# Performance work log

Hardware: AMD Instinct MI355X
Metric: run time of the kernel (lower is better)

The kernel has to match this reference:

```python
import jax, jax.numpy as jnp
import numpy as np

B, N, D, H, LH, AH = 4, 2048, 512, 4, 64, 64
NUM_BUCKETS = 128
EPS = 1e-6
LENGTHS = np.array([2048, 1536, 1024, 1792])  # jagged per-sequence lengths, sum = 6400


def _ln(x, eps=EPS):
    # F.layer_norm without affine params (biased variance)
    m = jnp.mean(x, axis=-1, keepdims=True)
    v = jnp.var(x, axis=-1, keepdims=True)
    return (x - m) * jax.lax.rsqrt(v + eps)


def _rel_bias(all_timestamps, ts_w):
    # bucketed time-delta relative attention bias -> [B, N, N]
    delta = (all_timestamps[:, :, None] - all_timestamps[:, None, :]).astype(jnp.float32)
    bucket = jnp.clip(jnp.floor(jnp.log1p(jnp.abs(delta))).astype(jnp.int32), 0, NUM_BUCKETS)
    return ts_w[bucket]


def setup_inputs() -> dict:
    key = jax.random.key(0)
    ks = jax.random.split(key, 6)
    offsets = np.concatenate([[0], np.cumsum(LENGTHS)]).astype(np.int32)
    T = int(offsets[-1])
    token_batch = np.repeat(np.arange(B), LENGTHS).astype(np.int32)
    token_pos = np.concatenate([np.arange(l) for l in LENGTHS]).astype(np.int32)
    x = jax.random.normal(ks[0], (T, D), jnp.float32)
    uvqk = jax.random.normal(ks[1], (D, 2 * LH * H + 2 * AH * H), jnp.float32) * 0.02
    o_w = jax.random.normal(ks[2], (D, LH * H), jnp.float32) * 0.02  # torch Linear weight [out, in]
    o_b = jnp.zeros((D,), jnp.float32)
    ts_w = jax.random.normal(ks[3], (NUM_BUCKETS + 1,), jnp.float32) * 0.02
    all_timestamps = jnp.sort(jax.random.randint(ks[4], (B, N), 0, 1000000, jnp.int32), axis=-1)
    invalid_attn_mask = jnp.tril(jnp.ones((N, N), jnp.float32))  # causal validity mask in {0,1}
    return {
        'x': x, 'uvqk': uvqk, 'o_w': o_w, 'o_b': o_b, 'ts_w': ts_w,
        'all_timestamps': all_timestamps, 'invalid_attn_mask': invalid_attn_mask,
        'x_offsets': jnp.asarray(offsets), 'token_batch': jnp.asarray(token_batch),
        'token_pos': jnp.asarray(token_pos),
    }


def reference(x, uvqk, o_w, o_b, ts_w, all_timestamps, invalid_attn_mask,
              x_offsets, token_batch, token_pos):
    # input layernorm + fused uvqk projection with SiLU
    h = jax.nn.silu(_ln(x) @ uvqk)  # [T, 2*H*LH + 2*H*AH]
    u, v, q, k = jnp.split(h, [LH * H, 2 * LH * H, 2 * LH * H + AH * H], axis=1)

    def pad(vals):  # jagged [T, d] -> padded dense [B, N, d]
        return jnp.zeros((B, N, vals.shape[-1]), vals.dtype).at[token_batch, token_pos].set(vals)

    pq = pad(q).reshape(B, N, H, AH)
    pk = pad(k).reshape(B, N, H, AH)
    pv = pad(v).reshape(B, N, H, LH)

    scores = jnp.einsum('bnhd,bmhd->bhnm', pq, pk)
    scores = scores + _rel_bias(all_timestamps, ts_w)[:, None]  # broadcast over heads
    scores = jax.nn.silu(scores) / N
    scores = scores * invalid_attn_mask[None, None]
    attn = jnp.einsum('bhnm,bmhd->bnhd', scores, pv).reshape(B, N, H * LH)
    attn_j = attn[token_batch, token_pos]  # dense -> jagged [T, H*LH]

    o_in = u * _ln(attn_j)
    return o_in @ o_w.T + o_b + x
```

## Files before the change

### kernel.cpp

```cpp
#include <hip/hip_runtime.h>
#include <math.h>


typedef __attribute__((ext_vector_type(8))) short bf16x8;
typedef __attribute__((ext_vector_type(4))) float f32x4;

__device__ __forceinline__ float silu_over_2048(float v) {
    return v * __builtin_amdgcn_rcpf(2048.0f + 2048.0f * __expf(-v));
}

__device__ __forceinline__ float silu_f(float v) {
    return v * __builtin_amdgcn_rcpf(1.0f + __expf(-v));
}

__device__ __forceinline__ unsigned short f2bf(float f) {
    unsigned int u = __float_as_uint(f);
    u += 0x7fffu + ((u >> 16) & 1u);
    return (unsigned short)(u >> 16);
}

__device__ __forceinline__ unsigned int f2bf2(float lo, float hi) {
#if __has_builtin(__builtin_amdgcn_cvt_pk_bf16_f32)
    typedef __attribute__((ext_vector_type(2))) short bf16x2;
    bf16x2 p = __builtin_amdgcn_cvt_pk_bf16_f32(lo, hi);
    return *(unsigned int*)&p;
#else
    return (unsigned int)f2bf(lo) | ((unsigned int)f2bf(hi) << 16);
#endif
}

__device__ __forceinline__ void gload_lds16(const unsigned short* g, unsigned short* l) {
    __builtin_amdgcn_global_load_lds(
        (const __attribute__((address_space(1))) void*)(g),
        (__attribute__((address_space(3))) void*)(l),
        16, 0, 0);
}

__global__ __launch_bounds__(256) void k1_ln_prep(const float* __restrict__ x,
                                                  unsigned short* __restrict__ xnb,
                                                  const float* __restrict__ uvqk,
                                                  unsigned short* __restrict__ uvqkT,
                                                  const float* __restrict__ ow,
                                                  unsigned short* __restrict__ owb) {
    const int tid = threadIdx.x;
    const int bx = blockIdx.x;
    if (bx < 1600) {
        const int row = bx * 4 + (tid >> 6);
        const int lane = tid & 63;
        const float* xr = x + row * 512 + lane * 8;
        const float4 v0 = *(const float4*)xr;
        const float4 v1 = *(const float4*)(xr + 4);
        float s = v0.x + v0.y + v0.z + v0.w + v1.x + v1.y + v1.z + v1.w;
        float ss = v0.x * v0.x + v0.y * v0.y + v0.z * v0.z + v0.w * v0.w +
                   v1.x * v1.x + v1.y * v1.y + v1.z * v1.z + v1.w * v1.w;
#pragma unroll
        for (int off = 32; off > 0; off >>= 1) {
            s += __shfl_down(s, off);
            ss += __shfl_down(ss, off);
        }
        s = __shfl(s, 0);
        ss = __shfl(ss, 0);
        const float mean = s * (1.0f / 512.0f);
        const float var = ss * (1.0f / 512.0f) - mean * mean;
        const float rstd = rsqrtf(var + 1e-6f);
        unsigned int pk[4];
        pk[0] = f2bf2((v0.x - mean) * rstd, (v0.y - mean) * rstd);
        pk[1] = f2bf2((v0.z - mean) * rstd, (v0.w - mean) * rstd);
        pk[2] = f2bf2((v1.x - mean) * rstd, (v1.y - mean) * rstd);
        pk[3] = f2bf2((v1.z - mean) * rstd, (v1.w - mean) * rstd);
        *(uint4*)(xnb + row * 512 + lane * 8) = *(const uint4*)pk;
    } else if (bx < 1728) {
        __shared__ float L[64][68];
        const int t = bx - 1600;
        const int n0 = (t & 15) * 64;
        const int k0 = (t >> 4) * 64;
#pragma unroll
        for (int i = 0; i < 4; ++i) {
            const int r = (tid >> 4) + i * 16;
            const int c = (tid & 15) * 4;
            *(float4*)&L[r][c] = *(const float4*)(uvqk + (k0 + r) * 1024 + n0 + c);
        }
        __syncthreads();
        const int n = tid >> 2;
        const int kb = (tid & 3) * 16;
#pragma unroll
        for (int pass = 0; pass < 2; ++pass) {
            unsigned short pk[8];
#pragma unroll
            for (int j = 0; j < 8; ++j) pk[j] = f2bf(L[kb + pass * 8 + j][n]);
            *(uint4*)(uvqkT + (n0 + n) * 512 + k0 + kb + pass * 8) = *(const uint4*)pk;
        }
    } else {
        const int base = ((bx - 1728) * 256 + tid) * 8;
        float4 a = *(const float4*)(ow + base);
        float4 b = *(const float4*)(ow + base + 4);
        unsigned short pk[8] = {f2bf(a.x), f2bf(a.y), f2bf(a.z), f2bf(a.w),
                                f2bf(b.x), f2bf(b.y), f2bf(b.z), f2bf(b.w)};
        *(uint4*)(owb + base) = *(const uint4*)pk;
    }
}

__global__ __launch_bounds__(256, 4) void k2_gemm1(const unsigned short* __restrict__ A,
                                                   const unsigned short* __restrict__ Bt,
                                                   float* __restrict__ u_out,
                                                   unsigned short* __restrict__ hb,
                                                   unsigned short* __restrict__ vtb) {
    __shared__ __align__(16) unsigned short smem[8192];
    unsigned short* As = smem;
    unsigned short* Bs = smem + 4096;
    const int tid = threadIdx.x;
    const int lane = tid & 63;
    const int w = tid >> 6;
    const int l15 = lane & 15;
    const int quad = lane >> 4;
    const int bm = blockIdx.y * 64;
    const int bn = blockIdx.x * 64;

    const int srow = lane >> 3;
    const int scol = ((lane & 7) ^ srow) * 8;
    const unsigned short* gA = A + (size_t)(bm + w * 8 + srow) * 512 + scol;
    const unsigned short* gB = Bt + (size_t)(bn + w * 8 + srow) * 512 + scol;

    const int xA = (l15 & 7) << 3;
    f32x4 acc[4] = {};
    for (int kc = 0; kc < 512; kc += 64) {
        __syncthreads();
#pragma unroll
        for (int i = 0; i < 2; ++i) {
            gload_lds16(gA + (size_t)(i * 32) * 512 + kc, As + (w + i * 4) * 512);
            gload_lds16(gB + (size_t)(i * 32) * 512 + kc, Bs + (w + i * 4) * 512);
        }
        __syncthreads();
        const bf16x8 a0 = *(const bf16x8*)&As[(w * 16 + l15) * 64 + ((quad * 8) ^ xA)];
        const bf16x8 a1 = *(const bf16x8*)&As[(w * 16 + l15) * 64 + ((32 + quad * 8) ^ xA)];
#pragma unroll
        for (int nt = 0; nt < 4; ++nt) {
            bf16x8 b0 = *(const bf16x8*)&Bs[(nt * 16 + l15) * 64 + ((quad * 8) ^ xA)];
            bf16x8 b1 = *(const bf16x8*)&Bs[(nt * 16 + l15) * 64 + ((32 + quad * 8) ^ xA)];
            acc[nt] = __builtin_amdgcn_mfma_f32_16x16x32_bf16(a0, b0, acc[nt], 0, 0, 0);
            acc[nt] = __builtin_amdgcn_mfma_f32_16x16x32_bf16(a1, b1, acc[nt], 0, 0, 0);
        }
    }
    const int m = bm + w * 16 + quad * 4;
    if (bn < 256) {
#pragma unroll
        for (int nt = 0; nt < 4; ++nt)
#pragma unroll
            for (int reg = 0; reg < 4; ++reg)
                __builtin_nontemporal_store(silu_f(acc[nt][reg]),
                                            &u_out[(m + reg) * 256 + bn + nt * 16 + l15]);
    } else if (bn < 512) {
        unsigned short(*T)[72] = (unsigned short(*)[72])smem;
        __syncthreads();
#pragma unroll
        for (int nt = 0; nt < 4; ++nt) {
            unsigned int p01 = f2bf2(silu_f(acc[nt][0]), silu_f(acc[nt][1]));
            unsigned int p23 = f2bf2(silu_f(acc[nt][2]), silu_f(acc[nt][3]));
            unsigned int pk2[2] = {p01, p23};
            *(uint2*)&T[nt * 16 + l15][w * 16 + quad * 4] = *(const uint2*)pk2;
        }
        __syncthreads();
        const int sr = tid >> 3, sc2 = (tid & 7) * 8;
#pragma unroll
        for (int i = 0; i < 2; ++i) {
            const int r = sr + i * 32;
            *(uint4*)(vtb + (size_t)(bn - 256 + r) * 6400 + bm + sc2) = *(const uint4*)&T[r][sc2];
        }
    } else {
        unsigned short(*T)[72] = (unsigned short(*)[72])smem;
        __syncthreads();
#pragma unroll
        for (int nt = 0; nt < 4; ++nt) {
            unsigned int p01 = f2bf2(silu_f(acc[nt][0]), silu_f(acc[nt][1]));
            unsigned int p23 = f2bf2(silu_f(acc[nt][2]), silu_f(acc[nt][3]));
            T[w * 16 + quad * 4 + 0][nt * 16 + l15] = (unsigned short)p01;
            T[w * 16 + quad * 4 + 1][nt * 16 + l15] = (unsigned short)(p01 >> 16);
            T[w * 16 + quad * 4 + 2][nt * 16 + l15] = (unsigned short)p23;
            T[w * 16 + quad * 4 + 3][nt * 16 + l15] = (unsigned short)(p23 >> 16);
        }
        __syncthreads();
        const int sr = tid >> 3, sc2 = (tid & 7) * 8;
#pragma unroll
        for (int i = 0; i < 2; ++i) {
            const int r = sr + i * 32;
            *(uint4*)(hb + (size_t)(bm + r) * 768 + (bn - 256) + sc2) = *(const uint4*)&T[r][sc2];
        }
    }
}

__global__ __launch_bounds__(256, 5) void k3_attn(const unsigned short* __restrict__ hb,
                                                  const unsigned short* __restrict__ vtb,
                                                  const int* __restrict__ ts,
                                                  const float* __restrict__ tsw,
                                                  const int* __restrict__ offs,
                                                  float* __restrict__ part) {
    const int xcd = blockIdx.x & 7;
    const int slot = blockIdx.x >> 3;
    const int b = (xcd < 3) ? 0 : (xcd < 5) ? 1 : (xcd == 5) ? 2 : 3;
    const int xst = (b == 0) ? 0 : (b == 1) ? 3 : (b == 2) ? 5 : 6;
    const int kx = (b == 0) ? 3 : (b == 2) ? 1 : 2;
    const int r = slot * kx + (xcd - xst);
    const int off = offs[b];
    const int len = offs[b + 1] - off;
    const int nqt = len >> 6;
    const int qt_lpt = r >> 5;
    if (qt_lpt >= nqt) return;
    const int qt = nqt - 1 - qt_lpt;
    const int c = (r >> 2) & 7;
    const int hd = r & 3;
    if (c * 4 > qt) return;
    const int q0 = qt * 64;
    const int kt_lo = c * 4;
    const int kt_hi = min(qt, c * 4 + 3);

    __shared__ __align__(16) unsigned short QPs[64][72];
    __shared__ __align__(16) unsigned short Ks[4096];
    __shared__ __align__(16) unsigned short Vt[4096];
    __shared__ float tqf[64], tkf[64];
    __shared__ float tw[132];

    const int tid = threadIdx.x;
    const int lane = tid & 63;
    const int w = tid >> 6;
    const int l15 = lane & 15;
    const int quad = lane >> 4;
    const int sr = tid >> 3;
    const int sc = (tid & 7) * 8;

    const int srow = lane >> 3;
    const int scol = ((lane & 7) ^ srow) * 8;
    const int xA = (l15 & 7) << 3;

    if (tid < 129) tw[tid] = tsw[tid];
    if (tid < 64) tqf[tid] = (float)ts[b * 2048 + q0 + tid];
#pragma unroll
    for (int i = 0; i < 2; ++i)
        *(uint4*)&QPs[sr + i * 32][sc] =
            *(const uint4*)(hb + (off + q0 + sr + i * 32) * 768 + 256 + hd * 64 + sc);
    __syncthreads();

    const bf16x8 aQ0 = *(const bf16x8*)&QPs[w * 16 + l15][quad * 8];
    const bf16x8 aQ1 = *(const bf16x8*)&QPs[w * 16 + l15][32 + quad * 8];
    const f32x4 tq4 = *(const f32x4*)&tqf[w * 16 + quad * 4];
    const int nbase = q0 + w * 16 + quad * 4;

    const unsigned short* gK = hb + (size_t)(off + w * 8 + srow) * 768 + 512 + hd * 64 + scol;
    const unsigned short* gV = vtb + (size_t)(hd * 64 + w * 8 + srow) * 6400 + off + scol;

    f32x4 oacc[4] = {};

    for (int kt = kt_lo; kt <= kt_hi; ++kt) {
        const int m0 = kt * 64;
        __syncthreads();
#pragma unroll
        for (int i = 0; i < 2; ++i) {
            gload_lds16(gK + (size_t)(m0 + i * 32) * 768, Ks + (w + i * 4) * 512);
            gload_lds16(gV + (size_t)(i * 32) * 6400 + m0, Vt + (w + i * 4) * 512);
        }
        if (tid < 64) tkf[tid] = (float)ts[b * 2048 + m0 + tid];
        __syncthreads();

        f32x4 s[4] = {};
#pragma unroll
        for (int nt = 0; nt < 4; ++nt) {
            bf16x8 b0 = *(const bf16x8*)&Ks[(nt * 16 + l15) * 64 + ((quad * 8) ^ xA)];
            bf16x8 b1 = *(const bf16x8*)&Ks[(nt * 16 + l15) * 64 + ((32 + quad * 8) ^ xA)];
            s[nt] = __builtin_amdgcn_mfma_f32_16x16x32_bf16(aQ0, b0, s[nt], 0, 0, 0);
            s[nt] = __builtin_amdgcn_mfma_f32_16x16x32_bf16(aQ1, b1, s[nt], 0, 0, 0);
        }

        const bool diag = (kt == qt);
#pragma unroll
        for (int nt = 0; nt < 4; ++nt) {
            const int m = m0 + nt * 16 + l15;
            const float tk = tkf[nt * 16 + l15];
            float p[4];
#pragma unroll
            for (int reg = 0; reg < 4; ++reg) {
                const float delta = fabsf(tq4[reg] - tk);
                const int bucket = (int)(__log2f(1.0f + delta) * 0.6931471805599453f);
                float val = s[nt][reg] + tw[bucket];
                float pv = silu_over_2048(val);
                if (diag) pv = (m <= nbase + reg) ? pv : 0.0f;
                p[reg] = pv;
            }
            const unsigned int p01 = f2bf2(p[0], p[1]);
            const unsigned int p23 = f2bf2(p[2], p[3]);
            QPs[w * 16 + quad * 4 + 0][nt * 16 + l15] = (unsigned short)p01;
            QPs[w * 16 + quad * 4 + 1][nt * 16 + l15] = (unsigned short)(p01 >> 16);
            QPs[w * 16 + quad * 4 + 2][nt * 16 + l15] = (unsigned short)p23;
            QPs[w * 16 + quad * 4 + 3][nt * 16 + l15] = (unsigned short)(p23 >> 16);
        }

        const bf16x8 aP0 = *(const bf16x8*)&QPs[w * 16 + l15][quad * 8];
        const bf16x8 aP1 = *(const bf16x8*)&QPs[w * 16 + l15][32 + quad * 8];
#pragma unroll
        for (int nt = 0; nt < 4; ++nt) {
            bf16x8 v0 = *(const bf16x8*)&Vt[(nt * 16 + l15) * 64 + ((quad * 8) ^ xA)];
            bf16x8 v1 = *(const bf16x8*)&Vt[(nt * 16 + l15) * 64 + ((32 + quad * 8) ^ xA)];
            oacc[nt] = __builtin_amdgcn_mfma_f32_16x16x32_bf16(aP0, v0, oacc[nt], 0, 0, 0);
            oacc[nt] = __builtin_amdgcn_mfma_f32_16x16x32_bf16(aP1, v1, oacc[nt], 0, 0, 0);
        }
    }

    float* pc = part + (size_t)c * (6400 * 256);
#pragma unroll
    for (int nt = 0; nt < 4; ++nt)
#pragma unroll
        for (int reg = 0; reg < 4; ++reg)
            __builtin_nontemporal_store(
                oacc[nt][reg],
                &pc[(off + q0 + w * 16 + quad * 4 + reg) * 256 + hd * 64 + nt * 16 + l15]);
}

__global__ __launch_bounds__(256) void k4a_ln(const float* __restrict__ part,
                                              const float* __restrict__ u_in,
                                              const int* __restrict__ token_pos,
                                              unsigned short* __restrict__ o_in) {
    const int row = blockIdx.x * 4 + (threadIdx.x >> 6);
    const int lane = threadIdx.x & 63;
    const int qt = token_pos[row] >> 6;
    const int nch = (qt + 4) >> 2;
    const size_t base = (size_t)row * 256 + lane * 4;
    f32x4 a = {0.0f, 0.0f, 0.0f, 0.0f};
    for (int cc = 0; cc < nch; ++cc) {
        const f32x4 p =
            __builtin_nontemporal_load((const f32x4*)(part + (size_t)cc * (6400 * 256) + base));
        a += p;
    }
    float s = a[0] + a[1] + a[2] + a[3];
    float ss = a[0] * a[0] + a[1] * a[1] + a[2] * a[2] + a[3] * a[3];
#pragma unroll
    for (int off = 32; off > 0; off >>= 1) {
        s += __shfl_down(s, off);
        ss += __shfl_down(ss, off);
    }
    s = __shfl(s, 0);
    ss = __shfl(ss, 0);
    const float mean = s * (1.0f / 256.0f);
    const float var = ss * (1.0f / 256.0f) - mean * mean;
    const float rstd = rsqrtf(var + 1e-6f);
    const f32x4 uu = __builtin_nontemporal_load((const f32x4*)(u_in + base));
    unsigned int pk[2];
    pk[0] = f2bf2(uu[0] * (a[0] - mean) * rstd, uu[1] * (a[1] - mean) * rstd);
    pk[1] = f2bf2(uu[2] * (a[2] - mean) * rstd, uu[3] * (a[3] - mean) * rstd);
    *(uint2*)(o_in + base) = *(const uint2*)pk;
}

__global__ __launch_bounds__(256, 4) void k4b_gemm2(const unsigned short* __restrict__ A,
                                                    const unsigned short* __restrict__ owb,
                                                    const float* __restrict__ ob,
                                                    const float* __restrict__ x,
                                                    float* __restrict__ out) {
    __shared__ __align__(16) unsigned short smem[8192];
    unsigned short* As = smem;
    unsigned short* Bs = smem + 4096;
    const int tid = threadIdx.x;
    const int lane = tid & 63;
    const int w = tid >> 6;
    const int l15 = lane & 15;
    const int quad = lane >> 4;
    const int bm = blockIdx.y * 64;
    const int bn = blockIdx.x * 64;

    const int srow = lane >> 3;
    const int scol = ((lane & 7) ^ srow) * 8;
    const unsigned short* gA = A + (size_t)(bm + w * 8 + srow) * 256 + scol;
    const unsigned short* gB = owb + (size_t)(bn + w * 8 + srow) * 256 + scol;

    const int xA = (l15 & 7) << 3;
    f32x4 acc[4] = {};
    for (int kc = 0; kc < 256; kc += 64) {
        __syncthreads();
#pragma unroll
        for (int i = 0; i < 2; ++i) {
            gload_lds16(gA + (size_t)(i * 32) * 256 + kc, As + (w + i * 4) * 512);
            gload_lds16(gB + (size_t)(i * 32) * 256 + kc, Bs + (w + i * 4) * 512);
        }
        __syncthreads();
        const bf16x8 a0 = *(const bf16x8*)&As[(w * 16 + l15) * 64 + ((quad * 8) ^ xA)];
        const bf16x8 a1 = *(const bf16x8*)&As[(w * 16 + l15) * 64 + ((32 + quad * 8) ^ xA)];
#pragma unroll
        for (int nt = 0; nt < 4; ++nt) {
            bf16x8 b0 = *(const bf16x8*)&Bs[(nt * 16 + l15) * 64 + ((quad * 8) ^ xA)];
            bf16x8 b1 = *(const bf16x8*)&Bs[(nt * 16 + l15) * 64 + ((32 + quad * 8) ^ xA)];
            acc[nt] = __builtin_amdgcn_mfma_f32_16x16x32_bf16(a0, b0, acc[nt], 0, 0, 0);
            acc[nt] = __builtin_amdgcn_mfma_f32_16x16x32_bf16(a1, b1, acc[nt], 0, 0, 0);
        }
    }
    const int m = bm + w * 16 + quad * 4;
#pragma unroll
    for (int nt = 0; nt < 4; ++nt) {
        const int d = bn + nt * 16 + l15;
        const float bias = ob[d];
#pragma unroll
        for (int reg = 0; reg < 4; ++reg)
            out[(m + reg) * 512 + d] = acc[nt][reg] + bias + x[(m + reg) * 512 + d];
    }
}

extern "C" void kernel_launch(void* const* d_in, const int* in_sizes, int n_in,
                              void* d_out, int out_size, void* d_ws, size_t ws_size,
                              hipStream_t stream) {
    const float* x = (const float*)d_in[0];
    const float* uvqk = (const float*)d_in[1];
    const float* ow = (const float*)d_in[2];
    const float* ob = (const float*)d_in[3];
    const float* tsw = (const float*)d_in[4];
    const int* ts = (const int*)d_in[5];
    const int* offs = (const int*)d_in[7];
    const int* token_pos = (const int*)d_in[9];
    float* out = (float*)d_out;

    float* ws = (float*)d_ws;
    float* u = ws;
    float* part = u + 6400 * 256;
    unsigned short* xnb = (unsigned short*)(part + 8 * 6400 * 256);
    unsigned short* hb = xnb + 6400 * 512;
    unsigned short* o_in = hb + 6400 * 768;
    unsigned short* uvqkT = o_in + 6400 * 256;
    unsigned short* owb = uvqkT + 1024 * 512;
    unsigned short* vtb = owb + 512 * 256;

    k1_ln_prep<<<1792, 256, 0, stream>>>(x, xnb, uvqk, uvqkT, ow, owb);
    k2_gemm1<<<dim3(16, 100), 256, 0, stream>>>(xnb, uvqkT, u, hb, vtb);
    k3_attn<<<4096, 256, 0, stream>>>(hb, vtb, ts, tsw, offs, part);
    k4a_ln<<<1600, 256, 0, stream>>>(part, u, token_pos, o_in);
    k4b_gemm2<<<dim3(8, 100), 256, 0, stream>>>(o_in, owb, ob, x, out);
}
```

Before: 146.7 us.

## Widen gemm1 tiles to 64x128 and remap GEMM blocks across XCDs

```diff
diff --git a/kernel.cpp b/kernel.cpp
--- a/kernel.cpp
+++ b/kernel.cpp
@@ -105,85 +105,108 @@
                                                    float* __restrict__ u_out,
                                                    unsigned short* __restrict__ hb,
                                                    unsigned short* __restrict__ vtb) {
-    __shared__ __align__(16) unsigned short smem[8192];
+    __shared__ __align__(16) unsigned short smem[12288];
     unsigned short* As = smem;
-    unsigned short* Bs = smem + 4096;
+    unsigned short* Bs0 = smem + 4096;
+    unsigned short* Bs1 = smem + 8192;
     const int tid = threadIdx.x;
     const int lane = tid & 63;
     const int w = tid >> 6;
     const int l15 = lane & 15;
     const int quad = lane >> 4;
-    const int bm = blockIdx.y * 64;
-    const int bn = blockIdx.x * 64;
+    const int bid = blockIdx.x;
+    const int kk_ = (bid & 7) * 100 + (bid >> 3);
+    const int bm = (kk_ >> 3) * 64;
+    const int bn0 = (kk_ & 7) * 128;
 
     const int srow = lane >> 3;
     const int scol = ((lane & 7) ^ srow) * 8;
     const unsigned short* gA = A + (size_t)(bm + w * 8 + srow) * 512 + scol;
-    const unsigned short* gB = Bt + (size_t)(bn + w * 8 + srow) * 512 + scol;
+    const unsigned short* gB0 = Bt + (size_t)(bn0 + w * 8 + srow) * 512 + scol;
+    const unsigned short* gB1 = Bt + (size_t)(bn0 + 64 + w * 8 + srow) * 512 + scol;
 
     const int xA = (l15 & 7) << 3;
-    f32x4 acc[4] = {};
+    f32x4 acc[2][4] = {};
     for (int kc = 0; kc < 512; kc += 64) {
         __syncthreads();
 #pragma unroll
         for (int i = 0; i < 2; ++i) {
             gload_lds16(gA + (size_t)(i * 32) * 512 + kc, As + (w + i * 4) * 512);
-            gload_lds16(gB + (size_t)(i * 32) * 512 + kc, Bs + (w + i * 4) * 512);
+            gload_lds16(gB0 + (size_t)(i * 32) * 512 + kc, Bs0 + (w + i * 4) * 512);
+            gload_lds16(gB1 + (size_t)(i * 32) * 512 + kc, Bs1 + (w + i * 4) * 512);
         }
         __syncthreads();
         const bf16x8 a0 = *(const bf16x8*)&As[(w * 16 + l15) * 64 + ((quad * 8) ^ xA)];
         const bf16x8 a1 = *(const bf16x8*)&As[(w * 16 + l15) * 64 + ((32 + quad * 8) ^ xA)];
 #pragma unroll
         for (int nt = 0; nt < 4; ++nt) {
-            bf16x8 b0 = *(const bf16x8*)&Bs[(nt * 16 + l15) * 64 + ((quad * 8) ^ xA)];
-            bf16x8 b1 = *(const bf16x8*)&Bs[(nt * 16 + l15) * 64 + ((32 + quad * 8) ^ xA)];
-            acc[nt] = __builtin_amdgcn_mfma_f32_16x16x32_bf16(a0, b0, acc[nt], 0, 0, 0);
-            acc[nt] = __builtin_amdgcn_mfma_f32_16x16x32_bf16(a1, b1, acc[nt], 0, 0, 0);
+            bf16x8 b0 = *(const bf16x8*)&Bs0[(nt * 16 + l15) * 64 + ((quad * 8) ^ xA)];
+            bf16x8 b1 = *(const bf16x8*)&Bs0[(nt * 16 + l15) * 64 + ((32 + quad * 8) ^ xA)];
+            acc[0][nt] = __builtin_amdgcn_mfma_f32_16x16x32_bf16(a0, b0, acc[0][nt], 0, 0, 0);
+            acc[0][nt] = __builtin_amdgcn_mfma_f32_16x16x32_bf16(a1, b1, acc[0][nt], 0, 0, 0);
+        }
+#pragma unroll
+        for (int nt = 0; nt < 4; ++nt) {
+            bf16x8 b0 = *(const bf16x8*)&Bs1[(nt * 16 + l15) * 64 + ((quad * 8) ^ xA)];
+            bf16x8 b1 = *(const bf16x8*)&Bs1[(nt * 16 + l15) * 64 + ((32 + quad * 8) ^ xA)];
+            acc[1][nt] = __builtin_amdgcn_mfma_f32_16x16x32_bf16(a0, b0, acc[1][nt], 0, 0, 0);
+            acc[1][nt] = __builtin_amdgcn_mfma_f32_16x16x32_bf16(a1, b1, acc[1][nt], 0, 0, 0);
         }
     }
     const int m = bm + w * 16 + quad * 4;
-    if (bn < 256) {
-#pragma unroll
-        for (int nt = 0; nt < 4; ++nt)
-#pragma unroll
-            for (int reg = 0; reg < 4; ++reg)
-                __builtin_nontemporal_store(silu_f(acc[nt][reg]),
-                                            &u_out[(m + reg) * 256 + bn + nt * 16 + l15]);
-    } else if (bn < 512) {
+    if (bn0 < 256) {
+#pragma unroll
+        for (int p = 0; p < 2; ++p)
+#pragma unroll
+            for (int nt = 0; nt < 4; ++nt)
+#pragma unroll
+                for (int reg = 0; reg < 4; ++reg)
+                    __builtin_nontemporal_store(
+                        silu_f(acc[p][nt][reg]),
+                        &u_out[(m + reg) * 256 + bn0 + p * 64 + nt * 16 + l15]);
+    } else if (bn0 < 512) {
         unsigned short(*T)[72] = (unsigned short(*)[72])smem;
-        __syncthreads();
-#pragma unroll
-        for (int nt = 0; nt < 4; ++nt) {
-            unsigned int p01 = f2bf2(silu_f(acc[nt][0]), silu_f(acc[nt][1]));
-            unsigned int p23 = f2bf2(silu_f(acc[nt][2]), silu_f(acc[nt][3]));
-            unsigned int pk2[2] = {p01, p23};
-            *(uint2*)&T[nt * 16 + l15][w * 16 + quad * 4] = *(const uint2*)pk2;
-        }
-        __syncthreads();
-        const int sr = tid >> 3, sc2 = (tid & 7) * 8;
-#pragma unroll
-        for (int i = 0; i < 2; ++i) {
-            const int r = sr + i * 32;
-            *(uint4*)(vtb + (size_t)(bn - 256 + r) * 6400 + bm + sc2) = *(const uint4*)&T[r][sc2];
+#pragma unroll
+        for (int p = 0; p < 2; ++p) {
+            __syncthreads();
+#pragma unroll
+            for (int nt = 0; nt < 4; ++nt) {
+                unsigned int p01 = f2bf2(silu_f(acc[p][nt][0]), silu_f(acc[p][nt][1]));
+                unsigned int p23 = f2bf2(silu_f(acc[p][nt][2]), silu_f(acc[p][nt][3]));
+                unsigned int pk2[2] = {p01, p23};
+                *(uint2*)&T[nt * 16 + l15][w * 16 + quad * 4] = *(const uint2*)pk2;
+            }
+            __syncthreads();
+            const int sr = tid >> 3, sc2 = (tid & 7) * 8;
+#pragma unroll
+            for (int i = 0; i < 2; ++i) {
+                const int r = sr + i * 32;
+                *(uint4*)(vtb + (size_t)(bn0 - 256 + p * 64 + r) * 6400 + bm + sc2) =
+                    *(const uint4*)&T[r][sc2];
+            }
         }
     } else {
         unsigned short(*T)[72] = (unsigned short(*)[72])smem;
-        __syncthreads();
-#pragma unroll
-        for (int nt = 0; nt < 4; ++nt) {
-            unsigned int p01 = f2bf2(silu_f(acc[nt][0]), silu_f(acc[nt][1]));
-            unsigned int p23 = f2bf2(silu_f(acc[nt][2]), silu_f(acc[nt][3]));
-            T[w * 16 + quad * 4 + 0][nt * 16 + l15] = (unsigned short)p01;
-            T[w * 16 + quad * 4 + 1][nt * 16 + l15] = (unsigned short)(p01 >> 16);
-            T[w * 16 + quad * 4 + 2][nt * 16 + l15] = (unsigned short)p23;
-            T[w * 16 + quad * 4 + 3][nt * 16 + l15] = (unsigned short)(p23 >> 16);
-        }
-        __syncthreads();
-        const int sr = tid >> 3, sc2 = (tid & 7) * 8;
-#pragma unroll
-        for (int i = 0; i < 2; ++i) {
-            const int r = sr + i * 32;
-            *(uint4*)(hb + (size_t)(bm + r) * 768 + (bn - 256) + sc2) = *(const uint4*)&T[r][sc2];
+#pragma unroll
+        for (int p = 0; p < 2; ++p) {
+            __syncthreads();
+#pragma unroll
+            for (int nt = 0; nt < 4; ++nt) {
+                unsigned int p01 = f2bf2(silu_f(acc[p][nt][0]), silu_f(acc[p][nt][1]));
+                unsigned int p23 = f2bf2(silu_f(acc[p][nt][2]), silu_f(acc[p][nt][3]));
+                T[w * 16 + quad * 4 + 0][nt * 16 + l15] = (unsigned short)p01;
+                T[w * 16 + quad * 4 + 1][nt * 16 + l15] = (unsigned short)(p01 >> 16);
+                T[w * 16 + quad * 4 + 2][nt * 16 + l15] = (unsigned short)p23;
+                T[w * 16 + quad * 4 + 3][nt * 16 + l15] = (unsigned short)(p23 >> 16);
+            }
+            __syncthreads();
+            const int sr = tid >> 3, sc2 = (tid & 7) * 8;
+#pragma unroll
+            for (int i = 0; i < 2; ++i) {
+                const int r = sr + i * 32;
+                *(uint4*)(hb + (size_t)(bm + r) * 768 + (bn0 - 256) + p * 64 + sc2) =
+                    *(const uint4*)&T[r][sc2];
+            }
         }
     }
 }
@@ -360,8 +383,10 @@
     const int w = tid >> 6;
     const int l15 = lane & 15;
     const int quad = lane >> 4;
-    const int bm = blockIdx.y * 64;
-    const int bn = blockIdx.x * 64;
+    const int bid = blockIdx.x;
+    const int kk_ = (bid & 7) * 100 + (bid >> 3);
+    const int bm = (kk_ >> 3) * 64;
+    const int bn = (kk_ & 7) * 64;
 
     const int srow = lane >> 3;
     const int scol = ((lane & 7) ^ srow) * 8;
@@ -423,8 +448,8 @@
     unsigned short* vtb = owb + 512 * 256;
 
     k1_ln_prep<<<1792, 256, 0, stream>>>(x, xnb, uvqk, uvqkT, ow, owb);
-    k2_gemm1<<<dim3(16, 100), 256, 0, stream>>>(xnb, uvqkT, u, hb, vtb);
+    k2_gemm1<<<800, 256, 0, stream>>>(xnb, uvqkT, u, hb, vtb);
     k3_attn<<<4096, 256, 0, stream>>>(hb, vtb, ts, tsw, offs, part);
     k4a_ln<<<1600, 256, 0, stream>>>(part, u, token_pos, o_in);
-    k4b_gemm2<<<dim3(8, 100), 256, 0, stream>>>(o_in, owb, ob, x, out);
-}
+    k4b_gemm2<<<800, 256, 0, stream>>>(o_in, owb, ob, x, out);
+}
```

New measurement: 146.3 us. About the same (-0.3%).
